# Kernel optimization log

Measured on AMD Instinct MI355X. Metric: run time of the kernel, lower is better.

## Reference

```python
import jax, jax.numpy as jnp
import numpy as np

N_NODES = 20000
N_EDGES = 200000
N_FEAT = 2048   # number_of_labels
H1 = 512        # GATE_hidden_size_1
H2 = 30         # GATE_hidden_size_2


def setup_inputs() -> dict:
    key = jax.random.key(0)
    ks = jax.random.split(key, 6)
    s = 0.05
    features = jax.random.normal(ks[0], (N_NODES, N_FEAT), dtype=jnp.float32)
    edge_index = jax.random.randint(ks[1], (2, N_EDGES), 0, N_NODES)
    W1 = jax.random.normal(ks[2], (N_FEAT, H1), dtype=jnp.float32) * s
    att_src1 = jax.random.normal(ks[3], (H1,), dtype=jnp.float32) * s
    att_dst1 = jax.random.normal(ks[4], (H1,), dtype=jnp.float32) * s
    W2 = jax.random.normal(ks[5], (H1, H2), dtype=jnp.float32) * s
    return {"features": features, "edge_index": edge_index,
            "W1": W1, "att_src1": att_src1, "att_dst1": att_dst1, "W2": W2}


def _segment_softmax(e, seg, n):
    # softmax over edges grouped by destination node (every node has a self loop)
    m = jax.ops.segment_max(e, seg, num_segments=n)
    ex = jnp.exp(e - m[seg])
    den = jax.ops.segment_sum(ex, seg, num_segments=n)
    return ex / den[seg]


def _gat_propagate(xw, a_src, a_dst, src, dst, n):
    # STAGATE GATConv message: alpha = sigmoid(a_src[j] + a_dst[i]), segment-softmax, scatter-add
    e = jax.nn.sigmoid(a_src[src] + a_dst[dst])          # [E]
    coef = _segment_softmax(e, dst, n)                   # [E]
    msg = xw[src] * coef[:, None]                        # [E, C] gather + scale
    return jax.ops.segment_sum(msg, dst, num_segments=n)  # [N, C] scatter-add


def reference(features, edge_index, W1, att_src1, att_dst1, W2):
    n = features.shape[0]
    loops = jnp.arange(n, dtype=edge_index.dtype)
    src = jnp.concatenate([edge_index[0], loops])  # add_self_loops=True
    dst = jnp.concatenate([edge_index[1], loops])

    # conv1 (attention=True): computes and stores node-level attention logits
    xw1 = features @ W1                 # [N, H1]
    a1s = xw1 @ att_src1                # [N]
    a1d = xw1 @ att_dst1                # [N]
    h1 = jax.nn.elu(_gat_propagate(xw1, a1s, a1d, src, dst, n))

    # conv2 (attention=False): plain linear transform, no propagation
    h2 = h1 @ W2                        # [N, H2]
    norm = jnp.sqrt(jnp.sum(h2 * h2, axis=1, keepdims=True))
    h2 = h2 / jnp.maximum(norm, 1e-12)  # F.normalize(dim=1)

    # conv3: weight tied to W2^T, attention tied to conv1's logits
    xw3 = h2 @ W2.T                     # [N, H1]
    h3 = jax.nn.elu(_gat_propagate(xw3, a1s, a1d, src, dst, n))

    # conv4 (attention=False): weight tied to W1^T
    h4 = h3 @ W1.T                      # [N, N_FEAT]

    return jnp.mean((features - h4) ** 2)  # F.mse_loss
```

## Files before the change

kernel.cpp:

```cpp
#include <hip/hip_runtime.h>
#include <math.h>

#define N_NODES 20000
#define N_EDGESI 200000
#define E_TOT   220000
#define N_FEAT  2048
#define H1      512
#define H2      30

typedef __bf16 bf16x8 __attribute__((ext_vector_type(8)));
typedef float  floatx4 __attribute__((ext_vector_type(4)));

__device__ __forceinline__ void lds_barrier() {
    asm volatile("s_waitcnt lgkmcnt(0)" ::: "memory");
    __builtin_amdgcn_s_barrier();
}

__device__ __forceinline__ unsigned short f2bf(float f) {
    unsigned int u = __float_as_uint(f);
    unsigned int r = (u + 0x7FFF + ((u >> 16) & 1)) >> 16;
    return (unsigned short)r;
}
__device__ __forceinline__ float bf2f(unsigned short u) {
    return __uint_as_float(((unsigned int)u) << 16);
}
__device__ __forceinline__ unsigned int packtrunc(float a, float b) {
    return (__float_as_uint(a) >> 16) | (__float_as_uint(b) & 0xFFFF0000u);
}
__device__ __forceinline__ unsigned int packrne(float a, float b) {
    return (unsigned int)f2bf(a) | ((unsigned int)f2bf(b) << 16);
}

__global__ __launch_bounds__(256) void cvtW1(const float* __restrict__ W1,
                                             unsigned short* __restrict__ w1bf,
                                             unsigned short* __restrict__ w1tbf) {
    __shared__ float tile[32][33];
    const int bk = blockIdx.y * 32, bn = blockIdx.x * 32;
    const int tc = threadIdx.x & 31, tr = threadIdx.x >> 5;
    for (int r = tr; r < 32; r += 8) {
        float v = W1[(size_t)(bk + r) * H1 + bn + tc];
        w1bf[(size_t)(bk + r) * H1 + bn + tc] = f2bf(v);
        tile[r][tc] = v;
    }
    __syncthreads();
    for (int r = tr; r < 32; r += 8) {
        w1tbf[(size_t)(bn + r) * N_FEAT + bk + tc] = f2bf(tile[tc][r]);
    }
}

__global__ __launch_bounds__(256, 5) void gemm1_mfma(const float* __restrict__ A,
                                                     const unsigned short* __restrict__ Bt,
                                                     unsigned short* __restrict__ C,
                                                     const float* __restrict__ atts,
                                                     const float* __restrict__ attd,
                                                     float* __restrict__ a1s,
                                                     float* __restrict__ a1d) {
    __shared__ unsigned short As[2][64 * 40];
    __shared__ unsigned short Bs[2][128 * 40];
    const int blk = blockIdx.x;
    const int xcd = blk & 7, rr = blk >> 3;
    const int ntile = rr & 3, group = rr >> 2;
    const int stripe = group * 8 + xcd;
    if (stripe >= 313) return;
    const int bm = stripe * 64, bn = ntile * 128;
    const int t = threadIdx.x;
    const int lane = t & 63, w = t >> 6;
    const int wm = w >> 1, wn = w & 1;
    const int ln = lane & 15, qd = lane >> 4;
    const int r0 = t >> 2, cs = (t & 3) * 8;

    int gra = bm + r0;        if (gra > N_NODES - 1) gra = N_NODES - 1;
    const float* ap0 = A + (size_t)gra * N_FEAT + cs;
    const unsigned short* bp0 = Bt + (size_t)(bn + r0) * N_FEAT + cs;
    const unsigned short* bp1 = Bt + (size_t)(bn + r0 + 64) * N_FEAT + cs;

    floatx4 acc[2][4];
#pragma unroll
    for (int i = 0; i < 2; i++)
#pragma unroll
        for (int j = 0; j < 4; j++) acc[i][j] = (floatx4){0.f, 0.f, 0.f, 0.f};

    float4 pa00 = *(const float4*)(ap0);
    float4 pa01 = *(const float4*)(ap0 + 4);
    uint4  pb0  = *(const uint4*)(bp0);
    uint4  pb1  = *(const uint4*)(bp1);
    {
        uint4 pk0;
        pk0.x = packtrunc(pa00.x, pa00.y); pk0.y = packtrunc(pa00.z, pa00.w);
        pk0.z = packtrunc(pa01.x, pa01.y); pk0.w = packtrunc(pa01.z, pa01.w);
        *(uint4*)&As[0][r0 * 40 + cs] = pk0;
        *(uint4*)&Bs[0][r0 * 40 + cs] = pb0;
        *(uint4*)&Bs[0][(r0 + 64) * 40 + cs] = pb1;
    }
    pa00 = *(const float4*)(ap0 + 32);
    pa01 = *(const float4*)(ap0 + 36);
    pb0  = *(const uint4*)(bp0 + 32);
    pb1  = *(const uint4*)(bp1 + 32);
    lds_barrier();

    int cur = 0;
    for (int k0 = 0; k0 < N_FEAT; k0 += 32) {
        bf16x8 af[2], bfr[4];
        const unsigned short* Ab = &As[cur][(wm * 32 + ln) * 40 + qd * 8];
        const unsigned short* Bb = &Bs[cur][(wn * 64 + ln) * 40 + qd * 8];
#pragma unroll
        for (int i = 0; i < 2; i++) af[i]  = *(const bf16x8*)(const void*)(Ab + i * 16 * 40);
#pragma unroll
        for (int j = 0; j < 4; j++) bfr[j] = *(const bf16x8*)(const void*)(Bb + j * 16 * 40);
        if (k0 + 32 < N_FEAT) {
            uint4 pk0;
            pk0.x = packtrunc(pa00.x, pa00.y); pk0.y = packtrunc(pa00.z, pa00.w);
            pk0.z = packtrunc(pa01.x, pa01.y); pk0.w = packtrunc(pa01.z, pa01.w);
            const int nb = cur ^ 1;
            *(uint4*)&As[nb][r0 * 40 + cs] = pk0;
            *(uint4*)&Bs[nb][r0 * 40 + cs] = pb0;
            *(uint4*)&Bs[nb][(r0 + 64) * 40 + cs] = pb1;
            if (k0 + 64 < N_FEAT) {
                const int kn = k0 + 64;
                pa00 = *(const float4*)(ap0 + kn);
                pa01 = *(const float4*)(ap0 + kn + 4);
                pb0  = *(const uint4*)(bp0 + kn);
                pb1  = *(const uint4*)(bp1 + kn);
            }
        }
#pragma unroll
        for (int i = 0; i < 2; i++)
#pragma unroll
            for (int j = 0; j < 4; j++)
                acc[i][j] = __builtin_amdgcn_mfma_f32_16x16x32_bf16(af[i], bfr[j], acc[i][j], 0, 0, 0);
        if (k0 + 32 < N_FEAT) lds_barrier();
        cur ^= 1;
    }

#pragma unroll
    for (int i = 0; i < 2; i++)
#pragma unroll
        for (int j = 0; j < 4; j++)
#pragma unroll
            for (int p = 0; p < 4; p++) {
                int m = bm + wm * 32 + i * 16 + qd * 4 + p;
                if (m < N_NODES) {
                    int n = bn + wn * 64 + j * 16 + ln;
                    C[(size_t)m * H1 + n] = f2bf(acc[i][j][p]);
                }
            }
    float avs[4], avd[4];
#pragma unroll
    for (int j = 0; j < 4; j++) {
        int n = bn + wn * 64 + j * 16 + ln;
        avs[j] = atts[n];
        avd[j] = attd[n];
    }
#pragma unroll
    for (int i = 0; i < 2; i++)
#pragma unroll
        for (int p = 0; p < 4; p++) {
            float vs = 0.f, vd = 0.f;
#pragma unroll
            for (int j = 0; j < 4; j++) {
                vs += acc[i][j][p] * avs[j];
                vd += acc[i][j][p] * avd[j];
            }
#pragma unroll
            for (int msk = 1; msk < 16; msk <<= 1) {
                vs += __shfl_xor(vs, msk);
                vd += __shfl_xor(vd, msk);
            }
            if (ln == p) {
                int m = bm + wm * 32 + i * 16 + qd * 4 + p;
                if (m < N_NODES) {
                    unsafeAtomicAdd(a1s + m, vs);
                    unsafeAtomicAdd(a1d + m, vd);
                }
            }
        }
}

__global__ __launch_bounds__(256) void gemm4_mse(const unsigned short* __restrict__ A,
                                                 const unsigned short* __restrict__ B,
                                                 const float* __restrict__ F,
                                                 float* __restrict__ partial) {
    __shared__ unsigned short As[2][128 * 40];
    __shared__ unsigned short Bs[2][128 * 40];
    __shared__ float red[256];
    const int blk = blockIdx.x;
    const int xcd = blk & 7, rr = blk >> 3;
    const int ntile = rr & 15, group = rr >> 4;
    const int stripe = group * 8 + xcd;
    if (stripe >= 157) return;
    const int bm = stripe * 128, bn = ntile * 128;
    const int t = threadIdx.x;
    const int lane = t & 63, w = t >> 6;
    const int wm = w >> 1, wn = w & 1;
    const int ln = lane & 15, qd = lane >> 4;
    const int r0 = t >> 2, cs = (t & 3) * 8;

    int gr0 = bm + r0;        if (gr0 > N_NODES - 1) gr0 = N_NODES - 1;
    int gr1 = bm + r0 + 64;   if (gr1 > N_NODES - 1) gr1 = N_NODES - 1;
    const unsigned short* ap0 = A + (size_t)gr0 * H1 + cs;
    const unsigned short* ap1 = A + (size_t)gr1 * H1 + cs;
    const unsigned short* bp0 = B + (size_t)(bn + r0) * H1 + cs;
    const unsigned short* bp1 = B + (size_t)(bn + r0 + 64) * H1 + cs;

    floatx4 acc[4][4];
#pragma unroll
    for (int i = 0; i < 4; i++)
#pragma unroll
        for (int j = 0; j < 4; j++) acc[i][j] = (floatx4){0.f, 0.f, 0.f, 0.f};

    uint4 pa0 = *(const uint4*)(ap0);
    uint4 pa1 = *(const uint4*)(ap1);
    uint4 pb0 = *(const uint4*)(bp0);
    uint4 pb1 = *(const uint4*)(bp1);
    *(uint4*)&As[0][r0 * 40 + cs] = pa0;
    *(uint4*)&As[0][(r0 + 64) * 40 + cs] = pa1;
    *(uint4*)&Bs[0][r0 * 40 + cs] = pb0;
    *(uint4*)&Bs[0][(r0 + 64) * 40 + cs] = pb1;
    pa0 = *(const uint4*)(ap0 + 32);
    pa1 = *(const uint4*)(ap1 + 32);
    pb0 = *(const uint4*)(bp0 + 32);
    pb1 = *(const uint4*)(bp1 + 32);
    lds_barrier();

    int cur = 0;
    for (int k0 = 0; k0 < H1; k0 += 32) {
        bf16x8 af[4], bfr[4];
        const unsigned short* Ab = &As[cur][(wm * 64 + ln) * 40 + qd * 8];
        const unsigned short* Bb = &Bs[cur][(wn * 64 + ln) * 40 + qd * 8];
#pragma unroll
        for (int i = 0; i < 4; i++) af[i]  = *(const bf16x8*)(const void*)(Ab + i * 16 * 40);
#pragma unroll
        for (int j = 0; j < 4; j++) bfr[j] = *(const bf16x8*)(const void*)(Bb + j * 16 * 40);
        if (k0 + 32 < H1) {
            const int nb = cur ^ 1;
            *(uint4*)&As[nb][r0 * 40 + cs] = pa0;
            *(uint4*)&As[nb][(r0 + 64) * 40 + cs] = pa1;
            *(uint4*)&Bs[nb][r0 * 40 + cs] = pb0;
            *(uint4*)&Bs[nb][(r0 + 64) * 40 + cs] = pb1;
            if (k0 + 64 < H1) {
                const int kn = k0 + 64;
                pa0 = *(const uint4*)(ap0 + kn);
                pa1 = *(const uint4*)(ap1 + kn);
                pb0 = *(const uint4*)(bp0 + kn);
                pb1 = *(const uint4*)(bp1 + kn);
            }
        }
#pragma unroll
        for (int i = 0; i < 4; i++)
#pragma unroll
            for (int j = 0; j < 4; j++)
                acc[i][j] = __builtin_amdgcn_mfma_f32_16x16x32_bf16(af[i], bfr[j], acc[i][j], 0, 0, 0);
        if (k0 + 32 < H1) lds_barrier();
        cur ^= 1;
    }
    float sum = 0.f;
#pragma unroll
    for (int i = 0; i < 4; i++)
#pragma unroll
        for (int j = 0; j < 4; j++)
#pragma unroll
            for (int p = 0; p < 4; p++) {
                int m = bm + wm * 64 + i * 16 + qd * 4 + p;
                if (m < N_NODES) {
                    int n = bn + wn * 64 + j * 16 + ln;
                    float fv = F[(size_t)m * N_FEAT + n];
                    float d = fv - acc[i][j][p];
                    sum += d * d;
                }
            }
    red[t] = sum;
    __syncthreads();
    for (int off = 128; off; off >>= 1) {
        if (t < off) red[t] += red[t + off];
        __syncthreads();
    }
    if (t == 0) unsafeAtomicAdd(partial, red[0]);
}

__global__ void edge_att(const int* __restrict__ ei,
                         const float* __restrict__ a1s,
                         const float* __restrict__ a1d,
                         float* __restrict__ ebuf,
                         float* __restrict__ den,
                         int* __restrict__ deg) {
    int e = blockIdx.x * blockDim.x + threadIdx.x;
    if (e >= E_TOT) return;
    int s, d;
    if (e < N_EDGESI) { s = ei[e]; d = ei[N_EDGESI + e]; }
    else { s = e - N_EDGESI; d = s; }
    float x = a1s[s] + a1d[d];
    float sig = 1.f / (1.f + __expf(-x));
    float ex = __expf(sig);
    ebuf[e] = ex;
    unsafeAtomicAdd(&den[d], ex);
    atomicAdd(&deg[d], 1);
}

__global__ __launch_bounds__(1024) void scan_k(const int* __restrict__ deg,
                                               int* __restrict__ off) {
    __shared__ int wsum[16];
    __shared__ int carry_s;
    const int lane = threadIdx.x & 63, wid = threadIdx.x >> 6;
    if (threadIdx.x == 0) carry_s = 0;
    __syncthreads();
    for (int base = 0; base < N_NODES; base += 1024) {
        int i = base + threadIdx.x;
        int v = (i < N_NODES) ? deg[i] : 0;
        int x = v;
#pragma unroll
        for (int s = 1; s < 64; s <<= 1) {
            int tt = __shfl_up(x, s);
            if (lane >= s) x += tt;
        }
        if (lane == 63) wsum[wid] = x;
        __syncthreads();
        if (wid == 0 && lane < 16) {
            int wv = wsum[lane];
#pragma unroll
            for (int s = 1; s < 16; s <<= 1) {
                int tt = __shfl_up(wv, s);
                if (lane >= s) wv += tt;
            }
            wsum[lane] = wv;
        }
        __syncthreads();
        int wbase = (wid == 0) ? 0 : wsum[wid - 1];
        int c = carry_s;
        int incl = x + wbase + c;
        if (i < N_NODES) off[i] = incl - v;
        __syncthreads();
        if (threadIdx.x == 0) carry_s = c + wsum[15];
        __syncthreads();
    }
}

__global__ void bucket_k(const int* __restrict__ ei,
                         const float* __restrict__ ebuf,
                         const float* __restrict__ den,
                         int* __restrict__ cursor,
                         int* __restrict__ csr_src,
                         float* __restrict__ csr_coef) {
    int e = blockIdx.x * blockDim.x + threadIdx.x;
    if (e >= E_TOT) return;
    int s, d;
    if (e < N_EDGESI) { s = ei[e]; d = ei[N_EDGESI + e]; }
    else { s = e - N_EDGESI; d = s; }
    int pos = atomicAdd(&cursor[d], 1);
    csr_src[pos] = s;
    csr_coef[pos] = ebuf[e] / den[d];
}

__global__ __launch_bounds__(256) void gather_elu_bf(const int* __restrict__ off,
                                                     const int* __restrict__ csr_src,
                                                     const float* __restrict__ csr_coef,
                                                     const unsigned short* __restrict__ X,
                                                     unsigned short* __restrict__ Y) {
    int d = blockIdx.x * 4 + (threadIdx.x >> 6);
    int lane = threadIdx.x & 63;
    if (d >= N_NODES) return;
    int beg = off[d];
    int end = (d == N_NODES - 1) ? E_TOT : off[d + 1];
    float a[8] = {0.f, 0.f, 0.f, 0.f, 0.f, 0.f, 0.f, 0.f};
    float b[8] = {0.f, 0.f, 0.f, 0.f, 0.f, 0.f, 0.f, 0.f};
    int j = beg;
    for (; j + 1 < end; j += 2) {
        int s0 = csr_src[j], s1 = csr_src[j + 1];
        float c0 = csr_coef[j], c1 = csr_coef[j + 1];
        uint4 raw0 = *(const uint4*)(X + (size_t)s0 * H1 + lane * 8);
        uint4 raw1 = *(const uint4*)(X + (size_t)s1 * H1 + lane * 8);
        a[0] += __uint_as_float(raw0.x << 16) * c0;
        a[1] += __uint_as_float(raw0.x & 0xFFFF0000u) * c0;
        a[2] += __uint_as_float(raw0.y << 16) * c0;
        a[3] += __uint_as_float(raw0.y & 0xFFFF0000u) * c0;
        a[4] += __uint_as_float(raw0.z << 16) * c0;
        a[5] += __uint_as_float(raw0.z & 0xFFFF0000u) * c0;
        a[6] += __uint_as_float(raw0.w << 16) * c0;
        a[7] += __uint_as_float(raw0.w & 0xFFFF0000u) * c0;
        b[0] += __uint_as_float(raw1.x << 16) * c1;
        b[1] += __uint_as_float(raw1.x & 0xFFFF0000u) * c1;
        b[2] += __uint_as_float(raw1.y << 16) * c1;
        b[3] += __uint_as_float(raw1.y & 0xFFFF0000u) * c1;
        b[4] += __uint_as_float(raw1.z << 16) * c1;
        b[5] += __uint_as_float(raw1.z & 0xFFFF0000u) * c1;
        b[6] += __uint_as_float(raw1.w << 16) * c1;
        b[7] += __uint_as_float(raw1.w & 0xFFFF0000u) * c1;
    }
    if (j < end) {
        int s0 = csr_src[j];
        float c0 = csr_coef[j];
        uint4 raw0 = *(const uint4*)(X + (size_t)s0 * H1 + lane * 8);
        a[0] += __uint_as_float(raw0.x << 16) * c0;
        a[1] += __uint_as_float(raw0.x & 0xFFFF0000u) * c0;
        a[2] += __uint_as_float(raw0.y << 16) * c0;
        a[3] += __uint_as_float(raw0.y & 0xFFFF0000u) * c0;
        a[4] += __uint_as_float(raw0.z << 16) * c0;
        a[5] += __uint_as_float(raw0.z & 0xFFFF0000u) * c0;
        a[6] += __uint_as_float(raw0.w << 16) * c0;
        a[7] += __uint_as_float(raw0.w & 0xFFFF0000u) * c0;
    }
#pragma unroll
    for (int e = 0; e < 8; e++) {
        float v = a[e] + b[e];
        a[e] = v > 0.f ? v : __expf(v) - 1.f;
    }
    uint4 o;
    o.x = packrne(a[0], a[1]);
    o.y = packrne(a[2], a[3]);
    o.z = packrne(a[4], a[5]);
    o.w = packrne(a[6], a[7]);
    *(uint4*)(Y + (size_t)d * H1 + lane * 8) = o;
}

__global__ __launch_bounds__(256) void gemm2_norm_bf(const unsigned short* __restrict__ H1b,
                                                     const float* __restrict__ W2,
                                                     float* __restrict__ h2n) {
    __shared__ float hs[8 * 516];
    const int n0 = blockIdx.x * 8;
    const int tid = threadIdx.x;
    for (int idx = tid; idx < 512; idx += 256) {
        int r = idx >> 6, c = (idx & 63) * 8;
        uint4 raw = *(const uint4*)(H1b + (size_t)(n0 + r) * H1 + c);
        float* hp = hs + r * 516 + c;
        hp[0] = __uint_as_float(raw.x << 16);
        hp[1] = __uint_as_float(raw.x & 0xFFFF0000u);
        hp[2] = __uint_as_float(raw.y << 16);
        hp[3] = __uint_as_float(raw.y & 0xFFFF0000u);
        hp[4] = __uint_as_float(raw.z << 16);
        hp[5] = __uint_as_float(raw.z & 0xFFFF0000u);
        hp[6] = __uint_as_float(raw.w << 16);
        hp[7] = __uint_as_float(raw.w & 0xFFFF0000u);
    }
    __syncthreads();
    const int sub = tid >> 5, j = tid & 31;
    float a0 = 0.f, a1 = 0.f, a2 = 0.f, a3 = 0.f;
    if (j < H2) {
        const float* hr = hs + sub * 516;
        for (int k = 0; k < H1; k += 4) {
            a0 += hr[k] * W2[k * H2 + j];
            a1 += hr[k + 1] * W2[(k + 1) * H2 + j];
            a2 += hr[k + 2] * W2[(k + 2) * H2 + j];
            a3 += hr[k + 3] * W2[(k + 3) * H2 + j];
        }
    }
    float acc = (a0 + a1) + (a2 + a3);
    float sq = acc * acc;
    for (int m = 16; m; m >>= 1) sq += __shfl_xor(sq, m, 32);
    float inv = 1.f / fmaxf(sqrtf(sq), 1e-12f);
    if (j < H2) h2n[(size_t)(n0 + sub) * H2 + j] = acc * inv;
}

#define G3_CHUNK 40
__global__ __launch_bounds__(256) void gemm3_k(const float* __restrict__ h2n,
                                               const float* __restrict__ W2,
                                               unsigned short* __restrict__ xw3) {
    const int t = threadIdx.x;
    const int h0 = t << 1;
    float w0[H2], w1[H2];
#pragma unroll
    for (int k = 0; k < H2; k++) {
        w0[k] = W2[(size_t)h0 * H2 + k];
        w1[k] = W2[(size_t)h0 * H2 + H2 + k];
    }
    const int n0 = blockIdx.x * G3_CHUNK;
    const int nend = (n0 + G3_CHUNK < N_NODES) ? n0 + G3_CHUNK : N_NODES;
    for (int n = n0; n < nend; n++) {
        const float* hr = h2n + (size_t)n * H2;
        float a0 = 0.f, a1 = 0.f;
#pragma unroll
        for (int k = 0; k < H2; k++) {
            float hv = hr[k];
            a0 += hv * w0[k];
            a1 += hv * w1[k];
        }
        *(unsigned int*)(xw3 + (size_t)n * H1 + h0) = packrne(a0, a1);
    }
}

__global__ void finalize_k(const float* __restrict__ partial, float* __restrict__ out) {
    out[0] = partial[0] * (1.f / ((float)N_NODES * (float)N_FEAT));
}

extern "C" void kernel_launch(void* const* d_in, const int* in_sizes, int n_in,
                              void* d_out, int out_size, void* d_ws, size_t ws_size,
                              hipStream_t stream) {
    const float* features = (const float*)d_in[0];
    const int*   ei       = (const int*)d_in[1];
    const float* W1       = (const float*)d_in[2];
    const float* atts     = (const float*)d_in[3];
    const float* attd     = (const float*)d_in[4];
    const float* W2       = (const float*)d_in[5];
    float* out = (float*)d_out;

    char* ws = (char*)d_ws;
    unsigned short* xw1bf = (unsigned short*)(ws);
    unsigned short* h3bf  = (unsigned short*)(ws + 20480000);
    unsigned short* h1bf  = (unsigned short*)(ws + 40960000);
    unsigned short* w1bf  = (unsigned short*)(ws + 61440000);
    unsigned short* w1tbf = (unsigned short*)(ws + 63537152);
    float* h2n      = (float*)(ws + 65634304);
    float* a1s      = (float*)(ws + 68034304);
    float* a1d      = (float*)(ws + 68114304);
    float* den      = (float*)(ws + 68194304);
    int*   deg      = (int*)  (ws + 68274304);
    float* partial  = (float*)(ws + 68354304);
    float* ebuf     = (float*)(ws + 68354320);
    int*   off      = (int*)  (ws + 69234320);
    int*   cursor   = (int*)  (ws + 69314320);
    int*   csr_src  = (int*)  (ws + 69394320);
    float* csr_coef = (float*)(ws + 70274320);

    hipMemsetAsync(a1s, 0, 320016, stream);

    cvtW1<<<dim3(16, 64), 256, 0, stream>>>(W1, w1bf, w1tbf);

    gemm1_mfma<<<1280, 256, 0, stream>>>(features, w1tbf, xw1bf, atts, attd, a1s, a1d);

    edge_att<<<(E_TOT + 255) / 256, 256, 0, stream>>>(ei, a1s, a1d, ebuf, den, deg);

    scan_k<<<1, 1024, 0, stream>>>(deg, off);
    hipMemcpyAsync(cursor, off, 20000 * 4, hipMemcpyDeviceToDevice, stream);
    bucket_k<<<(E_TOT + 255) / 256, 256, 0, stream>>>(ei, ebuf, den, cursor, csr_src, csr_coef);

    gather_elu_bf<<<N_NODES / 4, 256, 0, stream>>>(off, csr_src, csr_coef, xw1bf, h1bf);

    gemm2_norm_bf<<<N_NODES / 8, 256, 0, stream>>>(h1bf, W2, h2n);

    gemm3_k<<<(N_NODES + G3_CHUNK - 1) / G3_CHUNK, 256, 0, stream>>>(h2n, W2, xw1bf);

    gather_elu_bf<<<N_NODES / 4, 256, 0, stream>>>(off, csr_src, csr_coef, xw1bf, h3bf);

    gemm4_mse<<<2560, 256, 0, stream>>>(h3bf, w1bf, features, partial);

    finalize_k<<<1, 1, 0, stream>>>(partial, out);
}
```

Baseline: 622.0 us.

## Expand MSE algebraically via Gram matrix to avoid full reconstruction GEMM

The loss is expanded as ||F||² - 2·tr(h3·xw1ᵀ) + h3·G·h3ᵀ, where G = W1ᵀW1 (512x512) is built by a small GEMM. ||F||² is accumulated inside gemm1 as the features are loaded, and the cross term reuses xw1. This replaces the 20000x2048x512 reconstruction GEMM that reread all features with a 20000x512x512 GEMM. The scan now writes the cursor directly, dropping a device memcpy. Partial sums move to double precision to limit cancellation error, though the bf16 G and h3 add some approximation.

New measurement: 598.9 us. 1.04x faster.

```diff
diff --git a/kernel.cpp b/kernel.cpp
--- a/kernel.cpp
+++ b/kernel.cpp
@@ -54,9 +54,11 @@
                                                      const float* __restrict__ atts,
                                                      const float* __restrict__ attd,
                                                      float* __restrict__ a1s,
-                                                     float* __restrict__ a1d) {
+                                                     float* __restrict__ a1d,
+                                                     double* __restrict__ pF2) {
     __shared__ unsigned short As[2][64 * 40];
     __shared__ unsigned short Bs[2][128 * 40];
+    __shared__ float red[256];
     const int blk = blockIdx.x;
     const int xcd = blk & 7, rr = blk >> 3;
     const int ntile = rr & 3, group = rr >> 2;
@@ -74,6 +76,9 @@
     const unsigned short* bp0 = Bt + (size_t)(bn + r0) * N_FEAT + cs;
     const unsigned short* bp1 = Bt + (size_t)(bn + r0 + 64) * N_FEAT + cs;
 
+    const bool fz = (ntile == 0) && (bm + r0 < N_NODES);
+    float fsum = 0.f;
+
     floatx4 acc[2][4];
 #pragma unroll
     for (int i = 0; i < 2; i++)
@@ -91,6 +96,10 @@
         *(uint4*)&As[0][r0 * 40 + cs] = pk0;
         *(uint4*)&Bs[0][r0 * 40 + cs] = pb0;
         *(uint4*)&Bs[0][(r0 + 64) * 40 + cs] = pb1;
+        if (fz) {
+            fsum += pa00.x * pa00.x + pa00.y * pa00.y + pa00.z * pa00.z + pa00.w * pa00.w;
+            fsum += pa01.x * pa01.x + pa01.y * pa01.y + pa01.z * pa01.z + pa01.w * pa01.w;
+        }
     }
     pa00 = *(const float4*)(ap0 + 32);
     pa01 = *(const float4*)(ap0 + 36);
@@ -115,6 +124,10 @@
             *(uint4*)&As[nb][r0 * 40 + cs] = pk0;
             *(uint4*)&Bs[nb][r0 * 40 + cs] = pb0;
             *(uint4*)&Bs[nb][(r0 + 64) * 40 + cs] = pb1;
+            if (fz) {
+                fsum += pa00.x * pa00.x + pa00.y * pa00.y + pa00.z * pa00.z + pa00.w * pa00.w;
+                fsum += pa01.x * pa01.x + pa01.y * pa01.y + pa01.z * pa01.z + pa01.w * pa01.w;
+            }
             if (k0 + 64 < N_FEAT) {
                 const int kn = k0 + 64;
                 pa00 = *(const float4*)(ap0 + kn);
@@ -174,107 +187,189 @@
                 }
             }
         }
-}
-
-__global__ __launch_bounds__(256) void gemm4_mse(const unsigned short* __restrict__ A,
-                                                 const unsigned short* __restrict__ B,
-                                                 const float* __restrict__ F,
-                                                 float* __restrict__ partial) {
-    __shared__ unsigned short As[2][128 * 40];
+    if (ntile == 0) {
+        red[t] = fsum;
+        __syncthreads();
+        for (int off = 128; off; off >>= 1) {
+            if (t < off) red[t] += red[t + off];
+            __syncthreads();
+        }
+        if (t == 0) unsafeAtomicAdd(pF2, (double)red[0]);
+    }
+}
+
+__global__ __launch_bounds__(256, 5) void gemmg_k(const unsigned short* __restrict__ Wt,
+                                                  unsigned short* __restrict__ G) {
+    __shared__ unsigned short As[2][64 * 40];
     __shared__ unsigned short Bs[2][128 * 40];
-    __shared__ float red[256];
-    const int blk = blockIdx.x;
-    const int xcd = blk & 7, rr = blk >> 3;
-    const int ntile = rr & 15, group = rr >> 4;
-    const int stripe = group * 8 + xcd;
-    if (stripe >= 157) return;
-    const int bm = stripe * 128, bn = ntile * 128;
+    const int stripe = blockIdx.x >> 2, ntile = blockIdx.x & 3;
+    const int bm = stripe * 64, bn = ntile * 128;
     const int t = threadIdx.x;
     const int lane = t & 63, w = t >> 6;
     const int wm = w >> 1, wn = w & 1;
     const int ln = lane & 15, qd = lane >> 4;
     const int r0 = t >> 2, cs = (t & 3) * 8;
 
-    int gr0 = bm + r0;        if (gr0 > N_NODES - 1) gr0 = N_NODES - 1;
-    int gr1 = bm + r0 + 64;   if (gr1 > N_NODES - 1) gr1 = N_NODES - 1;
-    const unsigned short* ap0 = A + (size_t)gr0 * H1 + cs;
-    const unsigned short* ap1 = A + (size_t)gr1 * H1 + cs;
-    const unsigned short* bp0 = B + (size_t)(bn + r0) * H1 + cs;
-    const unsigned short* bp1 = B + (size_t)(bn + r0 + 64) * H1 + cs;
-
-    floatx4 acc[4][4];
-#pragma unroll
-    for (int i = 0; i < 4; i++)
+    const unsigned short* ap0 = Wt + (size_t)(bm + r0) * N_FEAT + cs;
+    const unsigned short* bp0 = Wt + (size_t)(bn + r0) * N_FEAT + cs;
+    const unsigned short* bp1 = Wt + (size_t)(bn + r0 + 64) * N_FEAT + cs;
+
+    floatx4 acc[2][4];
+#pragma unroll
+    for (int i = 0; i < 2; i++)
 #pragma unroll
         for (int j = 0; j < 4; j++) acc[i][j] = (floatx4){0.f, 0.f, 0.f, 0.f};
 
-    uint4 pa0 = *(const uint4*)(ap0);
-    uint4 pa1 = *(const uint4*)(ap1);
+    uint4 pa  = *(const uint4*)(ap0);
     uint4 pb0 = *(const uint4*)(bp0);
     uint4 pb1 = *(const uint4*)(bp1);
-    *(uint4*)&As[0][r0 * 40 + cs] = pa0;
-    *(uint4*)&As[0][(r0 + 64) * 40 + cs] = pa1;
+    *(uint4*)&As[0][r0 * 40 + cs] = pa;
     *(uint4*)&Bs[0][r0 * 40 + cs] = pb0;
     *(uint4*)&Bs[0][(r0 + 64) * 40 + cs] = pb1;
-    pa0 = *(const uint4*)(ap0 + 32);
-    pa1 = *(const uint4*)(ap1 + 32);
+    pa  = *(const uint4*)(ap0 + 32);
     pb0 = *(const uint4*)(bp0 + 32);
     pb1 = *(const uint4*)(bp1 + 32);
     lds_barrier();
 
     int cur = 0;
+    for (int k0 = 0; k0 < N_FEAT; k0 += 32) {
+        bf16x8 af[2], bfr[4];
+        const unsigned short* Ab = &As[cur][(wm * 32 + ln) * 40 + qd * 8];
+        const unsigned short* Bb = &Bs[cur][(wn * 64 + ln) * 40 + qd * 8];
+#pragma unroll
+        for (int i = 0; i < 2; i++) af[i]  = *(const bf16x8*)(const void*)(Ab + i * 16 * 40);
+#pragma unroll
+        for (int j = 0; j < 4; j++) bfr[j] = *(const bf16x8*)(const void*)(Bb + j * 16 * 40);
+        if (k0 + 32 < N_FEAT) {
+            const int nb = cur ^ 1;
+            *(uint4*)&As[nb][r0 * 40 + cs] = pa;
+            *(uint4*)&Bs[nb][r0 * 40 + cs] = pb0;
+            *(uint4*)&Bs[nb][(r0 + 64) * 40 + cs] = pb1;
+            if (k0 + 64 < N_FEAT) {
+                const int kn = k0 + 64;
+                pa  = *(const uint4*)(ap0 + kn);
+                pb0 = *(const uint4*)(bp0 + kn);
+                pb1 = *(const uint4*)(bp1 + kn);
+            }
+        }
+#pragma unroll
+        for (int i = 0; i < 2; i++)
+#pragma unroll
+            for (int j = 0; j < 4; j++)
+                acc[i][j] = __builtin_amdgcn_mfma_f32_16x16x32_bf16(af[i], bfr[j], acc[i][j], 0, 0, 0);
+        if (k0 + 32 < N_FEAT) lds_barrier();
+        cur ^= 1;
+    }
+#pragma unroll
+    for (int i = 0; i < 2; i++)
+#pragma unroll
+        for (int j = 0; j < 4; j++)
+#pragma unroll
+            for (int p = 0; p < 4; p++) {
+                int m = bm + wm * 32 + i * 16 + qd * 4 + p;
+                int n = bn + wn * 64 + j * 16 + ln;
+                G[(size_t)m * H1 + n] = f2bf(acc[i][j][p]);
+            }
+}
+
+__global__ __launch_bounds__(256, 5) void gemmq_k(const unsigned short* __restrict__ Ah,
+                                                  const unsigned short* __restrict__ Gt,
+                                                  const unsigned short* __restrict__ XW1,
+                                                  double* __restrict__ pcross,
+                                                  double* __restrict__ pquad) {
+    __shared__ unsigned short As[2][64 * 40];
+    __shared__ unsigned short Bs[2][128 * 40];
+    __shared__ float2 red2[256];
+    const int blk = blockIdx.x;
+    const int xcd = blk & 7, rr = blk >> 3;
+    const int ntile = rr & 3, group = rr >> 2;
+    const int stripe = group * 8 + xcd;
+    if (stripe >= 313) return;
+    const int bm = stripe * 64, bn = ntile * 128;
+    const int t = threadIdx.x;
+    const int lane = t & 63, w = t >> 6;
+    const int wm = w >> 1, wn = w & 1;
+    const int ln = lane & 15, qd = lane >> 4;
+    const int r0 = t >> 2, cs = (t & 3) * 8;
+
+    int gra = bm + r0; if (gra > N_NODES - 1) gra = N_NODES - 1;
+    const unsigned short* ap0 = Ah + (size_t)gra * H1 + cs;
+    const unsigned short* bp0 = Gt + (size_t)(bn + r0) * H1 + cs;
+    const unsigned short* bp1 = Gt + (size_t)(bn + r0 + 64) * H1 + cs;
+
+    floatx4 acc[2][4];
+#pragma unroll
+    for (int i = 0; i < 2; i++)
+#pragma unroll
+        for (int j = 0; j < 4; j++) acc[i][j] = (floatx4){0.f, 0.f, 0.f, 0.f};
+
+    uint4 pa  = *(const uint4*)(ap0);
+    uint4 pb0 = *(const uint4*)(bp0);
+    uint4 pb1 = *(const uint4*)(bp1);
+    *(uint4*)&As[0][r0 * 40 + cs] = pa;
+    *(uint4*)&Bs[0][r0 * 40 + cs] = pb0;
+    *(uint4*)&Bs[0][(r0 + 64) * 40 + cs] = pb1;
+    pa  = *(const uint4*)(ap0 + 32);
+    pb0 = *(const uint4*)(bp0 + 32);
+    pb1 = *(const uint4*)(bp1 + 32);
+    lds_barrier();
+
+    int cur = 0;
     for (int k0 = 0; k0 < H1; k0 += 32) {
-        bf16x8 af[4], bfr[4];
-        const unsigned short* Ab = &As[cur][(wm * 64 + ln) * 40 + qd * 8];
+        bf16x8 af[2], bfr[4];
+        const unsigned short* Ab = &As[cur][(wm * 32 + ln) * 40 + qd * 8];
         const unsigned short* Bb = &Bs[cur][(wn * 64 + ln) * 40 + qd * 8];
 #pragma unroll
-        for (int i = 0; i < 4; i++) af[i]  = *(const bf16x8*)(const void*)(Ab + i * 16 * 40);
+        for (int i = 0; i < 2; i++) af[i]  = *(const bf16x8*)(const void*)(Ab + i * 16 * 40);
 #pragma unroll
         for (int j = 0; j < 4; j++) bfr[j] = *(const bf16x8*)(const void*)(Bb + j * 16 * 40);
         if (k0 + 32 < H1) {
             const int nb = cur ^ 1;
-            *(uint4*)&As[nb][r0 * 40 + cs] = pa0;
-            *(uint4*)&As[nb][(r0 + 64) * 40 + cs] = pa1;
+            *(uint4*)&As[nb][r0 * 40 + cs] = pa;
             *(uint4*)&Bs[nb][r0 * 40 + cs] = pb0;
             *(uint4*)&Bs[nb][(r0 + 64) * 40 + cs] = pb1;
             if (k0 + 64 < H1) {
                 const int kn = k0 + 64;
-                pa0 = *(const uint4*)(ap0 + kn);
-                pa1 = *(const uint4*)(ap1 + kn);
+                pa  = *(const uint4*)(ap0 + kn);
                 pb0 = *(const uint4*)(bp0 + kn);
                 pb1 = *(const uint4*)(bp1 + kn);
             }
         }
 #pragma unroll
-        for (int i = 0; i < 4; i++)
+        for (int i = 0; i < 2; i++)
 #pragma unroll
             for (int j = 0; j < 4; j++)
                 acc[i][j] = __builtin_amdgcn_mfma_f32_16x16x32_bf16(af[i], bfr[j], acc[i][j], 0, 0, 0);
         if (k0 + 32 < H1) lds_barrier();
         cur ^= 1;
     }
-    float sum = 0.f;
-#pragma unroll
-    for (int i = 0; i < 4; i++)
+
+    float qsum = 0.f, csum = 0.f;
+#pragma unroll
+    for (int i = 0; i < 2; i++)
 #pragma unroll
         for (int j = 0; j < 4; j++)
 #pragma unroll
             for (int p = 0; p < 4; p++) {
-                int m = bm + wm * 64 + i * 16 + qd * 4 + p;
+                int m = bm + wm * 32 + i * 16 + qd * 4 + p;
                 if (m < N_NODES) {
                     int n = bn + wn * 64 + j * 16 + ln;
-                    float fv = F[(size_t)m * N_FEAT + n];
-                    float d = fv - acc[i][j][p];
-                    sum += d * d;
+                    float h3v = bf2f(Ah[(size_t)m * H1 + n]);
+                    float xv  = bf2f(XW1[(size_t)m * H1 + n]);
+                    qsum += acc[i][j][p] * h3v;
+                    csum += xv * h3v;
                 }
             }
-    red[t] = sum;
+    red2[t].x = qsum; red2[t].y = csum;
     __syncthreads();
     for (int off = 128; off; off >>= 1) {
-        if (t < off) red[t] += red[t + off];
+        if (t < off) { red2[t].x += red2[t + off].x; red2[t].y += red2[t + off].y; }
         __syncthreads();
     }
-    if (t == 0) unsafeAtomicAdd(partial, red[0]);
+    if (t == 0) {
+        unsafeAtomicAdd(pquad,  (double)red2[0].x);
+        unsafeAtomicAdd(pcross, (double)red2[0].y);
+    }
 }
 
 __global__ void edge_att(const int* __restrict__ ei,
@@ -297,7 +392,8 @@
 }
 
 __global__ __launch_bounds__(1024) void scan_k(const int* __restrict__ deg,
-                                               int* __restrict__ off) {
+                                               int* __restrict__ off,
+                                               int* __restrict__ cursor) {
     __shared__ int wsum[16];
     __shared__ int carry_s;
     const int lane = threadIdx.x & 63, wid = threadIdx.x >> 6;
@@ -327,7 +423,7 @@
         int wbase = (wid == 0) ? 0 : wsum[wid - 1];
         int c = carry_s;
         int incl = x + wbase + c;
-        if (i < N_NODES) off[i] = incl - v;
+        if (i < N_NODES) { off[i] = incl - v; cursor[i] = incl - v; }
         __syncthreads();
         if (threadIdx.x == 0) carry_s = c + wsum[15];
         __syncthreads();
@@ -476,8 +572,9 @@
     }
 }
 
-__global__ void finalize_k(const float* __restrict__ partial, float* __restrict__ out) {
-    out[0] = partial[0] * (1.f / ((float)N_NODES * (float)N_FEAT));
+__global__ void finalize_k(const double* __restrict__ partial, float* __restrict__ out) {
+    out[0] = (float)((partial[0] - 2.0 * partial[1] + partial[2]) *
+                     (1.0 / ((double)N_NODES * (double)N_FEAT)));
 }
 
 extern "C" void kernel_launch(void* const* d_in, const int* in_sizes, int n_in,
@@ -498,38 +595,40 @@
     unsigned short* w1bf  = (unsigned short*)(ws + 61440000);
     unsigned short* w1tbf = (unsigned short*)(ws + 63537152);
     float* h2n      = (float*)(ws + 65634304);
-    float* a1s      = (float*)(ws + 68034304);
-    float* a1d      = (float*)(ws + 68114304);
-    float* den      = (float*)(ws + 68194304);
-    int*   deg      = (int*)  (ws + 68274304);
-    float* partial  = (float*)(ws + 68354304);
-    float* ebuf     = (float*)(ws + 68354320);
-    int*   off      = (int*)  (ws + 69234320);
-    int*   cursor   = (int*)  (ws + 69314320);
-    int*   csr_src  = (int*)  (ws + 69394320);
-    float* csr_coef = (float*)(ws + 70274320);
-
-    hipMemsetAsync(a1s, 0, 320016, stream);
+    unsigned short* Gbf = (unsigned short*)(ws + 65634304);
+    float*  a1s     = (float*) (ws + 68034304);
+    float*  a1d     = (float*) (ws + 68114304);
+    float*  den     = (float*) (ws + 68194304);
+    int*    deg     = (int*)   (ws + 68274304);
+    double* partial = (double*)(ws + 68354304);
+    float* ebuf     = (float*)(ws + 68354336);
+    int*   off      = (int*)  (ws + 69234336);
+    int*   cursor   = (int*)  (ws + 69314336);
+    int*   csr_src  = (int*)  (ws + 69394336);
+    float* csr_coef = (float*)(ws + 70274336);
+
+    hipMemsetAsync(a1s, 0, 320032, stream);
 
     cvtW1<<<dim3(16, 64), 256, 0, stream>>>(W1, w1bf, w1tbf);
 
-    gemm1_mfma<<<1280, 256, 0, stream>>>(features, w1tbf, xw1bf, atts, attd, a1s, a1d);
+    gemm1_mfma<<<1280, 256, 0, stream>>>(features, w1tbf, xw1bf, atts, attd, a1s, a1d, partial);
 
     edge_att<<<(E_TOT + 255) / 256, 256, 0, stream>>>(ei, a1s, a1d, ebuf, den, deg);
 
-    scan_k<<<1, 1024, 0, stream>>>(deg, off);
-    hipMemcpyAsync(cursor, off, 20000 * 4, hipMemcpyDeviceToDevice, stream);
+    scan_k<<<1, 1024, 0, stream>>>(deg, off, cursor);
     bucket_k<<<(E_TOT + 255) / 256, 256, 0, stream>>>(ei, ebuf, den, cursor, csr_src, csr_coef);
 
     gather_elu_bf<<<N_NODES / 4, 256, 0, stream>>>(off, csr_src, csr_coef, xw1bf, h1bf);
 
     gemm2_norm_bf<<<N_NODES / 8, 256, 0, stream>>>(h1bf, W2, h2n);
 
-    gemm3_k<<<(N_NODES + G3_CHUNK - 1) / G3_CHUNK, 256, 0, stream>>>(h2n, W2, xw1bf);
-
-    gather_elu_bf<<<N_NODES / 4, 256, 0, stream>>>(off, csr_src, csr_coef, xw1bf, h3bf);
-
-    gemm4_mse<<<2560, 256, 0, stream>>>(h3bf, w1bf, features, partial);
+    gemm3_k<<<(N_NODES + G3_CHUNK - 1) / G3_CHUNK, 256, 0, stream>>>(h2n, W2, h1bf);
+
+    gather_elu_bf<<<N_NODES / 4, 256, 0, stream>>>(off, csr_src, csr_coef, h1bf, h3bf);
+
+    gemmg_k<<<32, 256, 0, stream>>>(w1tbf, Gbf);
+
+    gemmq_k<<<1280, 256, 0, stream>>>(h3bf, Gbf, xw1bf, partial + 1, partial + 2);
 
     finalize_k<<<1, 1, 0, stream>>>(partial, out);
 }
```
